# Kernel tuning notes

Hardware: AMD Instinct MI355X
Metric: run time of the kernel (lower is better)

## Reference

```python
import jax, jax.numpy as jnp
import numpy as np

NUM_GROUPS = 32
EPS = 1e-6


def group_norm(x, gamma, beta):
    # x: [B, C, H, W]
    B, C, H, W = x.shape
    xg = x.reshape(B, NUM_GROUPS, C // NUM_GROUPS, H, W)
    mean = jnp.mean(xg, axis=(2, 3, 4), keepdims=True)
    var = jnp.var(xg, axis=(2, 3, 4), keepdims=True)
    xn = (xg - mean) * jax.lax.rsqrt(var + EPS)
    xn = xn.reshape(B, C, H, W)
    return xn * gamma[None, :, None, None] + beta[None, :, None, None]


def conv1x1(x, w, b):
    # x: [B, C, H, W], w: [Cout, Cin], b: [Cout]
    return jnp.einsum('bchw,dc->bdhw', x, w) + b[None, :, None, None]


def setup_inputs() -> dict:
    key = jax.random.key(0)
    ks = jax.random.split(key, 11)
    B, C, H, W = 4, 512, 64, 64
    s = 1.0 / np.sqrt(C)
    return {
        'x': jax.random.normal(ks[0], (B, C, H, W), dtype=jnp.float32),
        'gn_gamma': jnp.ones((C,), dtype=jnp.float32),
        'gn_beta': jnp.zeros((C,), dtype=jnp.float32),
        'wq': jax.random.normal(ks[1], (C, C), dtype=jnp.float32) * s,
        'bq': jax.random.normal(ks[2], (C,), dtype=jnp.float32) * 0.01,
        'wk': jax.random.normal(ks[3], (C, C), dtype=jnp.float32) * s,
        'bk': jax.random.normal(ks[4], (C,), dtype=jnp.float32) * 0.01,
        'wv': jax.random.normal(ks[5], (C, C), dtype=jnp.float32) * s,
        'bv': jax.random.normal(ks[6], (C,), dtype=jnp.float32) * 0.01,
        'wo': jax.random.normal(ks[7], (C, C), dtype=jnp.float32) * s,
        'bo': jax.random.normal(ks[8], (C,), dtype=jnp.float32) * 0.01,
    }


def reference(x, gn_gamma, gn_beta, wq, bq, wk, bk, wv, bv, wo, bo):
    B, C, H, W = x.shape
    h = group_norm(x, gn_gamma, gn_beta)
    q = conv1x1(h, wq, bq).reshape(B, C, H * W)  # [B, C, N]
    k = conv1x1(h, wk, bk).reshape(B, C, H * W)
    v = conv1x1(h, wv, bv).reshape(B, C, H * W)
    scale = jnp.asarray(C, x.dtype) ** -0.5
    # scores[b, i, j] = q_i . k_j
    scores = jnp.einsum('bci,bcj->bij', q, k) * scale  # [B, N, N]
    attn = jax.nn.softmax(scores, axis=2)
    # out[b, c, i] = sum_j v[b, c, j] * attn[b, i, j]
    out = jnp.einsum('bcj,bij->bci', v, attn).reshape(B, C, H, W)
    out = conv1x1(out, wo, bo)
    return x + out
```

## Files before the change

kernel.cpp:

```cpp
#include <hip/hip_runtime.h>

using uint = unsigned int;
typedef short bf16x8 __attribute__((ext_vector_type(8)));
typedef _Float16 f16x8 __attribute__((ext_vector_type(8)));
typedef float f32x4 __attribute__((ext_vector_type(4)));
typedef long i64;
typedef i64 i64x2 __attribute__((ext_vector_type(2)));

static constexpr int Cc = 512;
static constexpr int Nn = 4096;
static constexpr size_t NC = (size_t)Nn * Cc;
static constexpr size_t SN = (size_t)Nn * Nn;

__device__ __forceinline__ unsigned short f2bf(float f) {
    unsigned int u = __builtin_bit_cast(unsigned int, f);
    u = (u + 0x7fff + ((u >> 16) & 1)) >> 16;
    return (unsigned short)u;
}
__device__ __forceinline__ unsigned short f2h(float f) {
    _Float16 h = (_Float16)f;
    return __builtin_bit_cast(unsigned short, h);
}
__device__ __forceinline__ int perm64(int k) {
    return (k & ~63) | ((k & 0x18) << 1) | ((k & 0x20) >> 2) | (k & 7);
}

__device__ __forceinline__ void gll16(const void* g, void* l) {
    __builtin_amdgcn_global_load_lds(
        (const __attribute__((address_space(1))) void*)g,
        (__attribute__((address_space(3))) void*)l, 16, 0, 0);
}

__global__ void cvt_kernel(const float* __restrict__ in, unsigned short* __restrict__ out, int n4) {
    int i = blockIdx.x * blockDim.x + threadIdx.x;
    if (i < n4) {
        float4 v = ((const float4*)in)[i];
        out[i * 4 + 0] = f2bf(v.x);
        out[i * 4 + 1] = f2bf(v.y);
        out[i * 4 + 2] = f2bf(v.z);
        out[i * 4 + 3] = f2bf(v.w);
    }
}

__global__ void zero_kernel(float* __restrict__ p, int n4) {
    int i = blockIdx.x * blockDim.x + threadIdx.x;
    if (i < n4) ((float4*)p)[i] = make_float4(0.f, 0.f, 0.f, 0.f);
}

__global__ void gn_stats_kernel(const float* __restrict__ x, float* __restrict__ meanb,
                                float* __restrict__ rsb) {
    int bg = blockIdx.x;
    const float* slab = x + (size_t)bg * 16 * Nn;
    const float4* s4 = (const float4*)slab;
    int t = threadIdx.x;
    float s1 = 0.f, s2 = 0.f;
#pragma unroll 8
    for (int k = 0; k < 64; ++k) {
        float4 v = s4[k * 256 + t];
        s1 += v.x + v.y + v.z + v.w;
        s2 += v.x * v.x + v.y * v.y + v.z * v.z + v.w * v.w;
    }
#pragma unroll
    for (int o = 32; o > 0; o >>= 1) { s1 += __shfl_down(s1, o); s2 += __shfl_down(s2, o); }
    __shared__ float r1[4], r2[4];
    int wv_ = t >> 6, ln = t & 63;
    if (ln == 0) { r1[wv_] = s1; r2[wv_] = s2; }
    __syncthreads();
    if (t == 0) {
        float a1 = r1[0] + r1[1] + r1[2] + r1[3];
        float a2 = r2[0] + r2[1] + r2[2] + r2[3];
        float mean = a1 * (1.f / 65536.f);
        float var = a2 * (1.f / 65536.f) - mean * mean;
        meanb[bg] = mean;
        rsb[bg] = rsqrtf(var + 1e-6f);
    }
}

__global__ __launch_bounds__(256) void gn_norm_kernel(
    const float* __restrict__ x, const float* __restrict__ meanb, const float* __restrict__ rsb,
    const float* __restrict__ gamma, const float* __restrict__ beta,
    unsigned short* __restrict__ h_t) {
    __shared__ float tile[64][65];
    int n0 = blockIdx.x * 64, c0 = blockIdx.y * 64, b = blockIdx.z;
    int t = threadIdx.x;
    const float* xb = x + (size_t)b * Cc * Nn;
#pragma unroll
    for (int j = 0; j < 4; ++j) {
        int i = j * 256 + t;
        int c = i >> 4;
        int n4 = i & 15;
        int cg = c0 + c;
        float4 v = ((const float4*)(xb + (size_t)cg * Nn + n0))[n4];
        int g = cg >> 4;
        float mean = meanb[b * 32 + g], rs = rsb[b * 32 + g];
        float ga = gamma[cg] * rs;
        float be = beta[cg] - mean * ga;
        tile[n4 * 4 + 0][c] = v.x * ga + be;
        tile[n4 * 4 + 1][c] = v.y * ga + be;
        tile[n4 * 4 + 2][c] = v.z * ga + be;
        tile[n4 * 4 + 3][c] = v.w * ga + be;
    }
    __syncthreads();
    int n = t >> 2;
    int cpart = (t & 3) * 16;
    unsigned short o[16];
#pragma unroll
    for (int q = 0; q < 16; ++q) o[q] = f2bf(tile[n][cpart + q]);
    unsigned short* dst = h_t + (size_t)b * NC + (size_t)(n0 + n) * Cc + c0 + cpart;
    ((uint4*)dst)[0] = ((uint4*)o)[0];
    ((uint4*)dst)[1] = ((uint4*)o)[1];
}

template <int BM, int DT, int BIAS_MODE, int OUT_MODE, int HAS_RES>
__global__ __launch_bounds__(256, 2) void gemm_bt(
    const unsigned short* __restrict__ A, int lda, size_t sA,
    const unsigned short* __restrict__ Bt, int ldb, size_t sB,
    void* __restrict__ outp, int ldc, size_t sC,
    const float* __restrict__ bias,
    const float* __restrict__ res, size_t sR,
    int K, float alpha) {
    constexpr int MT = BM / 32;
    __shared__ unsigned short lA[BM * 64];
    __shared__ unsigned short lB[128 * 64];
    int z = blockIdx.z;
    A += (size_t)z * sA;
    Bt += (size_t)z * sB;
    int m0 = blockIdx.y * BM, n0 = blockIdx.x * 128;
    int t = threadIdx.x;
    int lane = t & 63, wave = t >> 6;
    int wm = wave >> 1, wn = wave & 1;
    int lo = lane & 15, quad = lane >> 4;

    f32x4 acc[MT][4];
#pragma unroll
    for (int a1 = 0; a1 < MT; ++a1)
#pragma unroll
        for (int a2 = 0; a2 < 4; ++a2) acc[a1][a2] = (f32x4){0.f, 0.f, 0.f, 0.f};

    for (int k0 = 0; k0 < K; k0 += 64) {
#pragma unroll
        for (int p = 0; p < MT; ++p) {
            int ci = p * 256 + t;
            int row = ci >> 3;
            int gs = (ci ^ row) & 7;
            gll16(A + (size_t)(m0 + row) * lda + k0 + gs * 8, &lA[(size_t)ci * 8]);
        }
#pragma unroll
        for (int p = 0; p < 4; ++p) {
            int ci = p * 256 + t;
            int row = ci >> 3;
            int gs = (ci ^ row) & 7;
            gll16(Bt + (size_t)(n0 + row) * ldb + k0 + gs * 8, &lB[(size_t)ci * 8]);
        }
        __syncthreads();
#pragma unroll
        for (int ks = 0; ks < 2; ++ks) {
            int G = quad + ks * 4;
            bf16x8 af[MT], bfr[4];
#pragma unroll
            for (int mt = 0; mt < MT; ++mt) {
                int R = wm * (BM / 2) + mt * 16 + lo;
                af[mt] = *(const bf16x8*)&lA[R * 64 + (((G ^ R) & 7) << 3)];
            }
#pragma unroll
            for (int nt = 0; nt < 4; ++nt) {
                int R = wn * 64 + nt * 16 + lo;
                bfr[nt] = *(const bf16x8*)&lB[R * 64 + (((G ^ R) & 7) << 3)];
            }
#pragma unroll
            for (int mt = 0; mt < MT; ++mt)
#pragma unroll
                for (int nt = 0; nt < 4; ++nt) {
                    if (DT == 0)
                        acc[mt][nt] = __builtin_amdgcn_mfma_f32_16x16x32_bf16(af[mt], bfr[nt], acc[mt][nt], 0, 0, 0);
                    else
                        acc[mt][nt] = __builtin_amdgcn_mfma_f32_16x16x32_f16(
                            __builtin_bit_cast(f16x8, af[mt]), __builtin_bit_cast(f16x8, bfr[nt]),
                            acc[mt][nt], 0, 0, 0);
                }
        }
        __syncthreads();
    }

    size_t zc = (size_t)z * sC;
    float* outf = (float*)outp + zc;
    unsigned short* outb = (unsigned short*)outp + zc;
    unsigned char* outc = (unsigned char*)outp + zc;
    const float* resz = HAS_RES ? res + (size_t)z * sR : nullptr;

#pragma unroll
    for (int mt = 0; mt < MT; ++mt) {
#pragma unroll
        for (int nt = 0; nt < 4; ++nt) {
            int row = m0 + wm * (BM / 2) + mt * 16 + quad * 4;
            int col = n0 + wn * 64 + nt * 16 + lo;
            float bn = (BIAS_MODE == 2) ? bias[col] : 0.f;
#pragma unroll
            for (int r = 0; r < 4; ++r) {
                float vv = acc[mt][nt][r];
                if (BIAS_MODE == 1) vv += bias[row + r];
                if (BIAS_MODE == 2) vv += bn;
                vv *= alpha;
                if (OUT_MODE == 3) {
                    float e = fmaxf(fminf(vv, 448.f), -448.f);
                    int pk = __builtin_amdgcn_cvt_pk_fp8_f32(e, e, 0, false);
                    outc[(size_t)(row + r) * ldc + perm64(col)] = (unsigned char)(pk & 0xff);
                } else {
                    size_t off = (size_t)(row + r) * ldc + col;
                    if (HAS_RES) vv += resz[off];
                    if (OUT_MODE == 0) outf[off] = vv;
                    else if (OUT_MODE == 1) outb[off] = f2bf(vv);
                    else outb[off] = f2h(vv);
                }
            }
        }
    }
}

__global__ __launch_bounds__(256, 2) void qk_fp8(
    const unsigned char* __restrict__ Q, const unsigned char* __restrict__ Kt,
    unsigned char* __restrict__ S, float* __restrict__ lsum, float alpha) {
    __shared__ unsigned char lA[256 * 128];
    __shared__ unsigned char lB[128 * 128];
    int z = blockIdx.z;
    Q += (size_t)z * NC;
    Kt += (size_t)z * NC;
    S += (size_t)z * SN;
    lsum += (size_t)z * Nn;
    int m0 = blockIdx.y * 256, n0 = blockIdx.x * 128;
    int t = threadIdx.x;
    int lane = t & 63, wave = t >> 6;
    int wm = wave >> 1, wn = wave & 1;
    int lo = lane & 15, quad = lane >> 4;

    f32x4 acc[8][4];
#pragma unroll
    for (int a1 = 0; a1 < 8; ++a1)
#pragma unroll
        for (int a2 = 0; a2 < 4; ++a2) acc[a1][a2] = (f32x4){0.f, 0.f, 0.f, 0.f};

    for (int k0 = 0; k0 < Cc; k0 += 128) {
#pragma unroll
        for (int p = 0; p < 8; ++p) {
            int ci = p * 256 + t;
            int row = ci >> 3, g = ci & 7;
            int gs = g ^ (row & 7);
            gll16(Q + (size_t)(m0 + row) * Cc + k0 + gs * 16, &lA[ci * 16]);
        }
#pragma unroll
        for (int p = 0; p < 4; ++p) {
            int ci = p * 256 + t;
            int row = ci >> 3, g = ci & 7;
            int gs = g ^ (row & 7);
            gll16(Kt + (size_t)(n0 + row) * Cc + k0 + gs * 16, &lB[ci * 16]);
        }
        __syncthreads();
#pragma unroll
        for (int c = 0; c < 2; ++c) {
            int gb = c * 4 + quad;
            i64x2 aq[8], bq[4];
#pragma unroll
            for (int mt = 0; mt < 8; ++mt) {
                int R = wm * 128 + mt * 16 + lo;
                aq[mt] = *(const i64x2*)&lA[R * 128 + ((gb ^ (R & 7)) << 4)];
            }
#pragma unroll
            for (int nt = 0; nt < 4; ++nt) {
                int R = wn * 64 + nt * 16 + lo;
                bq[nt] = *(const i64x2*)&lB[R * 128 + ((gb ^ (R & 7)) << 4)];
            }
#pragma unroll
            for (int ks = 0; ks < 2; ++ks)
#pragma unroll
                for (int mt = 0; mt < 8; ++mt)
#pragma unroll
                    for (int nt = 0; nt < 4; ++nt)
                        acc[mt][nt] = __builtin_amdgcn_mfma_f32_16x16x32_fp8_fp8(
                            aq[mt][ks], bq[nt][ks], acc[mt][nt], 0, 0, 0);
        }
        __syncthreads();
    }

#pragma unroll
    for (int mt = 0; mt < 8; ++mt) {
        int row = m0 + wm * 128 + mt * 16 + quad * 4;
        float rsum[4] = {0.f, 0.f, 0.f, 0.f};
#pragma unroll
        for (int nt = 0; nt < 4; ++nt) {
            int col = n0 + wn * 64 + nt * 16 + lo;
            int colp = perm64(col);
#pragma unroll
            for (int r = 0; r < 4; ++r) {
                float e = __expf(acc[mt][nt][r] * alpha - 2.f);
                e = fminf(e, 448.f);
                int pk = __builtin_amdgcn_cvt_pk_fp8_f32(e, e, 0, false);
                S[(size_t)(row + r) * Nn + colp] = (unsigned char)(pk & 0xff);
                rsum[r] += __builtin_amdgcn_cvt_f32_fp8(pk, 0);
            }
        }
#pragma unroll
        for (int o = 1; o < 16; o <<= 1) {
#pragma unroll
            for (int r = 0; r < 4; ++r) rsum[r] += __shfl_xor(rsum[r], o);
        }
        if (lo == 0) {
#pragma unroll
            for (int r = 0; r < 4; ++r) atomicAdd(&lsum[row + r], rsum[r]);
        }
    }
}

__global__ __launch_bounds__(256, 3) void pv_fp8(
    const unsigned char* __restrict__ S, const unsigned char* __restrict__ V,
    const float* __restrict__ lsum, unsigned short* __restrict__ o_t) {
    __shared__ unsigned char lA[128 * 128];
    __shared__ unsigned char lB[128 * 128];
    int z = blockIdx.z;
    S += (size_t)z * SN;
    V += (size_t)z * NC;
    lsum += (size_t)z * Nn;
    o_t += (size_t)z * NC;
    int m0 = blockIdx.y * 128, n0 = blockIdx.x * 128;
    int t = threadIdx.x;
    int lane = t & 63, wave = t >> 6;
    int wm = wave >> 1, wn = wave & 1;
    int lo = lane & 15, quad = lane >> 4;

    f32x4 acc[4][4];
#pragma unroll
    for (int a1 = 0; a1 < 4; ++a1)
#pragma unroll
        for (int a2 = 0; a2 < 4; ++a2) acc[a1][a2] = (f32x4){0.f, 0.f, 0.f, 0.f};

    for (int k0 = 0; k0 < Nn; k0 += 128) {
#pragma unroll
        for (int p = 0; p < 4; ++p) {
            int ci = p * 256 + t;
            int row = ci >> 3, g = ci & 7;
            int gs = g ^ (row & 7);
            gll16(S + (size_t)(m0 + row) * Nn + k0 + gs * 16, &lA[ci * 16]);
        }
#pragma unroll
        for (int p = 0; p < 4; ++p) {
            int ci = p * 256 + t;
            int row = ci >> 3, g = ci & 7;
            int gs = g ^ (row & 7);
            gll16(V + (size_t)(n0 + row) * Nn + k0 + gs * 16, &lB[ci * 16]);
        }
        __syncthreads();
#pragma unroll
        for (int c = 0; c < 2; ++c) {
            int gb = c * 4 + quad;
            i64x2 aq[4], bq[4];
#pragma unroll
            for (int mt = 0; mt < 4; ++mt) {
                int R = wm * 64 + mt * 16 + lo;
                aq[mt] = *(const i64x2*)&lA[R * 128 + ((gb ^ (R & 7)) << 4)];
            }
#pragma unroll
            for (int nt = 0; nt < 4; ++nt) {
                int R = wn * 64 + nt * 16 + lo;
                bq[nt] = *(const i64x2*)&lB[R * 128 + ((gb ^ (R & 7)) << 4)];
            }
#pragma unroll
            for (int ks = 0; ks < 2; ++ks)
#pragma unroll
                for (int mt = 0; mt < 4; ++mt)
#pragma unroll
                    for (int nt = 0; nt < 4; ++nt)
                        acc[mt][nt] = __builtin_amdgcn_mfma_f32_16x16x32_fp8_fp8(
                            aq[mt][ks], bq[nt][ks], acc[mt][nt], 0, 0, 0);
        }
        __syncthreads();
    }

#pragma unroll
    for (int mt = 0; mt < 4; ++mt)
#pragma unroll
        for (int nt = 0; nt < 4; ++nt) {
            int row = m0 + wm * 64 + mt * 16 + quad * 4;
            int col = n0 + wn * 64 + nt * 16 + lo;
#pragma unroll
            for (int r = 0; r < 4; ++r) {
                float vv = acc[mt][nt][r] / lsum[row + r];
                o_t[(size_t)(row + r) * Cc + col] = f2bf(vv);
            }
        }
}

extern "C" void kernel_launch(void* const* d_in, const int* in_sizes, int n_in,
                              void* d_out, int out_size, void* d_ws, size_t ws_size,
                              hipStream_t stream) {
    const float* x     = (const float*)d_in[0];
    const float* gamma = (const float*)d_in[1];
    const float* beta  = (const float*)d_in[2];
    const float* wq = (const float*)d_in[3];
    const float* bq = (const float*)d_in[4];
    const float* wk = (const float*)d_in[5];
    const float* bk = (const float*)d_in[6];
    const float* wv = (const float*)d_in[7];
    const float* bv = (const float*)d_in[8];
    const float* wo = (const float*)d_in[9];
    const float* bo = (const float*)d_in[10];

    char* ws = (char*)d_ws;
    unsigned short* h_t  = (unsigned short*)(ws);
    unsigned char*  q_8  = (unsigned char*)(ws + 16777216);
    unsigned char*  k_8  = (unsigned char*)(ws + 33554432);
    unsigned char*  v_8  = (unsigned char*)(ws + 50331648);
    unsigned short* o_t  = (unsigned short*)(ws + 67108864);
    unsigned char*  S    = (unsigned char*)(ws + 83886080);
    unsigned short* wqb  = (unsigned short*)(ws + 218103808);
    unsigned short* wkb  = (unsigned short*)(ws + 218628096);
    unsigned short* wvb  = (unsigned short*)(ws + 219152384);
    unsigned short* wob  = (unsigned short*)(ws + 219676672);
    float* statm         = (float*)(ws + 220200960);
    float* statr         = (float*)(ws + 220201984);
    float* lsum          = (float*)(ws + 220203008);

    const float SCALE = 0.044194173824159216f;

    cvt_kernel<<<256, 256, 0, stream>>>(wq, wqb, 65536);
    cvt_kernel<<<256, 256, 0, stream>>>(wk, wkb, 65536);
    cvt_kernel<<<256, 256, 0, stream>>>(wv, wvb, 65536);
    cvt_kernel<<<256, 256, 0, stream>>>(wo, wob, 65536);
    zero_kernel<<<16, 256, 0, stream>>>(lsum, 4096);

    gn_stats_kernel<<<128, 256, 0, stream>>>(x, statm, statr);
    gn_norm_kernel<<<dim3(64, 8, 4), 256, 0, stream>>>(x, statm, statr, gamma, beta, h_t);

    gemm_bt<128, 0, 2, 3, 0><<<dim3(4, 32, 4), 256, 0, stream>>>(
        h_t, Cc, NC, wqb, Cc, 0, q_8, Cc, NC, bq, nullptr, 0, Cc, 1.f);
    gemm_bt<128, 0, 2, 3, 0><<<dim3(4, 32, 4), 256, 0, stream>>>(
        h_t, Cc, NC, wkb, Cc, 0, k_8, Cc, NC, bk, nullptr, 0, Cc, 1.f);
    gemm_bt<128, 0, 1, 3, 0><<<dim3(32, 4, 4), 256, 0, stream>>>(
        wvb, Cc, 0, h_t, Cc, NC, v_8, Nn, NC, bv, nullptr, 0, Cc, 1.f);

    qk_fp8<<<dim3(32, 16, 4), 256, 0, stream>>>(q_8, k_8, S, lsum, SCALE);
    pv_fp8<<<dim3(4, 32, 4), 256, 0, stream>>>(S, v_8, lsum, o_t);

    gemm_bt<128, 0, 1, 0, 1><<<dim3(32, 4, 4), 256, 0, stream>>>(
        wob, Cc, 0, o_t, Cc, NC, d_out, Nn, NC, bo, x, NC, Cc, 1.f);
}
```

Baseline: 314.9 us.

## Double-buffer LDS tiles in GEMM, QK and PV kernels to overlap loads

Converts the three matmul kernels to a two-stage LDS ping-pong: the next K-slice is issued via global-to-LDS loads while MFMAs run on the current buffer. The fp8 kernels shrink the K step from 128 to 64 bytes per stage so total LDS stays roughly the same, with a new XOR swizzle over 4 chunks. The aim is to hide global load latency behind compute. In exchange it doubles the iteration count and barrier count in the fp8 kernels, and the GEMM's LDS use doubles, which may reduce occupancy.

```diff
diff --git a/kernel.cpp b/kernel.cpp
--- a/kernel.cpp
+++ b/kernel.cpp
@@ -120,8 +120,8 @@
     const float* __restrict__ res, size_t sR,
     int K, float alpha) {
     constexpr int MT = BM / 32;
-    __shared__ unsigned short lA[BM * 64];
-    __shared__ unsigned short lB[128 * 64];
+    __shared__ unsigned short lA[2][BM * 64];
+    __shared__ unsigned short lB[2][128 * 64];
     int z = blockIdx.z;
     A += (size_t)z * sA;
     Bt += (size_t)z * sB;
@@ -137,22 +137,29 @@
 #pragma unroll
         for (int a2 = 0; a2 < 4; ++a2) acc[a1][a2] = (f32x4){0.f, 0.f, 0.f, 0.f};
 
-    for (int k0 = 0; k0 < K; k0 += 64) {
+    auto stage = [&](int buf, int k0) {
 #pragma unroll
         for (int p = 0; p < MT; ++p) {
             int ci = p * 256 + t;
             int row = ci >> 3;
             int gs = (ci ^ row) & 7;
-            gll16(A + (size_t)(m0 + row) * lda + k0 + gs * 8, &lA[(size_t)ci * 8]);
+            gll16(A + (size_t)(m0 + row) * lda + k0 + gs * 8, &lA[buf][ci * 8]);
         }
 #pragma unroll
         for (int p = 0; p < 4; ++p) {
             int ci = p * 256 + t;
             int row = ci >> 3;
             int gs = (ci ^ row) & 7;
-            gll16(Bt + (size_t)(n0 + row) * ldb + k0 + gs * 8, &lB[(size_t)ci * 8]);
-        }
-        __syncthreads();
+            gll16(Bt + (size_t)(n0 + row) * ldb + k0 + gs * 8, &lB[buf][ci * 8]);
+        }
+    };
+
+    int nk = K >> 6;
+    stage(0, 0);
+    __syncthreads();
+    int cur = 0;
+    for (int it = 0; it < nk; ++it) {
+        if (it + 1 < nk) stage(cur ^ 1, (it + 1) << 6);
 #pragma unroll
         for (int ks = 0; ks < 2; ++ks) {
             int G = quad + ks * 4;
@@ -160,12 +167,12 @@
 #pragma unroll
             for (int mt = 0; mt < MT; ++mt) {
                 int R = wm * (BM / 2) + mt * 16 + lo;
-                af[mt] = *(const bf16x8*)&lA[R * 64 + (((G ^ R) & 7) << 3)];
+                af[mt] = *(const bf16x8*)&lA[cur][R * 64 + (((G ^ R) & 7) << 3)];
             }
 #pragma unroll
             for (int nt = 0; nt < 4; ++nt) {
                 int R = wn * 64 + nt * 16 + lo;
-                bfr[nt] = *(const bf16x8*)&lB[R * 64 + (((G ^ R) & 7) << 3)];
+                bfr[nt] = *(const bf16x8*)&lB[cur][R * 64 + (((G ^ R) & 7) << 3)];
             }
 #pragma unroll
             for (int mt = 0; mt < MT; ++mt)
@@ -180,6 +187,7 @@
                 }
         }
         __syncthreads();
+        cur ^= 1;
     }
 
     size_t zc = (size_t)z * sC;
@@ -220,8 +228,8 @@
 __global__ __launch_bounds__(256, 2) void qk_fp8(
     const unsigned char* __restrict__ Q, const unsigned char* __restrict__ Kt,
     unsigned char* __restrict__ S, float* __restrict__ lsum, float alpha) {
-    __shared__ unsigned char lA[256 * 128];
-    __shared__ unsigned char lB[128 * 128];
+    __shared__ unsigned char lA[2][256 * 64];
+    __shared__ unsigned char lB[2][128 * 64];
     int z = blockIdx.z;
     Q += (size_t)z * NC;
     Kt += (size_t)z * NC;
@@ -239,46 +247,49 @@
 #pragma unroll
         for (int a2 = 0; a2 < 4; ++a2) acc[a1][a2] = (f32x4){0.f, 0.f, 0.f, 0.f};
 
-    for (int k0 = 0; k0 < Cc; k0 += 128) {
-#pragma unroll
-        for (int p = 0; p < 8; ++p) {
-            int ci = p * 256 + t;
-            int row = ci >> 3, g = ci & 7;
-            int gs = g ^ (row & 7);
-            gll16(Q + (size_t)(m0 + row) * Cc + k0 + gs * 16, &lA[ci * 16]);
-        }
+    auto stage = [&](int buf, int k0) {
 #pragma unroll
         for (int p = 0; p < 4; ++p) {
             int ci = p * 256 + t;
-            int row = ci >> 3, g = ci & 7;
-            int gs = g ^ (row & 7);
-            gll16(Kt + (size_t)(n0 + row) * Cc + k0 + gs * 16, &lB[ci * 16]);
-        }
+            int row = ci >> 2;
+            int gs = (ci ^ row) & 3;
+            gll16(Q + (size_t)(m0 + row) * Cc + k0 + gs * 16, &lA[buf][ci * 16]);
+        }
+#pragma unroll
+        for (int p = 0; p < 2; ++p) {
+            int ci = p * 256 + t;
+            int row = ci >> 2;
+            int gs = (ci ^ row) & 3;
+            gll16(Kt + (size_t)(n0 + row) * Cc + k0 + gs * 16, &lB[buf][ci * 16]);
+        }
+    };
+
+    stage(0, 0);
+    __syncthreads();
+    int cur = 0;
+    for (int it = 0; it < 8; ++it) {
+        if (it < 7) stage(cur ^ 1, (it + 1) * 64);
+        i64x2 aq[8], bq[4];
+#pragma unroll
+        for (int mt = 0; mt < 8; ++mt) {
+            int R = wm * 128 + mt * 16 + lo;
+            aq[mt] = *(const i64x2*)&lA[cur][R * 64 + ((quad ^ (R & 3)) << 4)];
+        }
+#pragma unroll
+        for (int nt = 0; nt < 4; ++nt) {
+            int R = wn * 64 + nt * 16 + lo;
+            bq[nt] = *(const i64x2*)&lB[cur][R * 64 + ((quad ^ (R & 3)) << 4)];
+        }
+#pragma unroll
+        for (int ks = 0; ks < 2; ++ks)
+#pragma unroll
+            for (int mt = 0; mt < 8; ++mt)
+#pragma unroll
+                for (int nt = 0; nt < 4; ++nt)
+                    acc[mt][nt] = __builtin_amdgcn_mfma_f32_16x16x32_fp8_fp8(
+                        aq[mt][ks], bq[nt][ks], acc[mt][nt], 0, 0, 0);
         __syncthreads();
-#pragma unroll
-        for (int c = 0; c < 2; ++c) {
-            int gb = c * 4 + quad;
-            i64x2 aq[8], bq[4];
-#pragma unroll
-            for (int mt = 0; mt < 8; ++mt) {
-                int R = wm * 128 + mt * 16 + lo;
-                aq[mt] = *(const i64x2*)&lA[R * 128 + ((gb ^ (R & 7)) << 4)];
-            }
-#pragma unroll
-            for (int nt = 0; nt < 4; ++nt) {
-                int R = wn * 64 + nt * 16 + lo;
-                bq[nt] = *(const i64x2*)&lB[R * 128 + ((gb ^ (R & 7)) << 4)];
-            }
-#pragma unroll
-            for (int ks = 0; ks < 2; ++ks)
-#pragma unroll
-                for (int mt = 0; mt < 8; ++mt)
-#pragma unroll
-                    for (int nt = 0; nt < 4; ++nt)
-                        acc[mt][nt] = __builtin_amdgcn_mfma_f32_16x16x32_fp8_fp8(
-                            aq[mt][ks], bq[nt][ks], acc[mt][nt], 0, 0, 0);
-        }
-        __syncthreads();
+        cur ^= 1;
     }
 
 #pragma unroll
@@ -313,8 +324,8 @@
 __global__ __launch_bounds__(256, 3) void pv_fp8(
     const unsigned char* __restrict__ S, const unsigned char* __restrict__ V,
     const float* __restrict__ lsum, unsigned short* __restrict__ o_t) {
-    __shared__ unsigned char lA[128 * 128];
-    __shared__ unsigned char lB[128 * 128];
+    __shared__ unsigned char lA[2][128 * 64];
+    __shared__ unsigned char lB[2][128 * 64];
     int z = blockIdx.z;
     S += (size_t)z * SN;
     V += (size_t)z * NC;
@@ -332,46 +343,49 @@
 #pragma unroll
         for (int a2 = 0; a2 < 4; ++a2) acc[a1][a2] = (f32x4){0.f, 0.f, 0.f, 0.f};
 
-    for (int k0 = 0; k0 < Nn; k0 += 128) {
-#pragma unroll
-        for (int p = 0; p < 4; ++p) {
-            int ci = p * 256 + t;
-            int row = ci >> 3, g = ci & 7;
-            int gs = g ^ (row & 7);
-            gll16(S + (size_t)(m0 + row) * Nn + k0 + gs * 16, &lA[ci * 16]);
-        }
-#pragma unroll
-        for (int p = 0; p < 4; ++p) {
-            int ci = p * 256 + t;
-            int row = ci >> 3, g = ci & 7;
-            int gs = g ^ (row & 7);
-            gll16(V + (size_t)(n0 + row) * Nn + k0 + gs * 16, &lB[ci * 16]);
-        }
+    auto stage = [&](int buf, int k0) {
+#pragma unroll
+        for (int p = 0; p < 2; ++p) {
+            int ci = p * 256 + t;
+            int row = ci >> 2;
+            int gs = (ci ^ row) & 3;
+            gll16(S + (size_t)(m0 + row) * Nn + k0 + gs * 16, &lA[buf][ci * 16]);
+        }
+#pragma unroll
+        for (int p = 0; p < 2; ++p) {
+            int ci = p * 256 + t;
+            int row = ci >> 2;
+            int gs = (ci ^ row) & 3;
+            gll16(V + (size_t)(n0 + row) * Nn + k0 + gs * 16, &lB[buf][ci * 16]);
+        }
+    };
+
+    stage(0, 0);
+    __syncthreads();
+    int cur = 0;
+    for (int it = 0; it < 64; ++it) {
+        if (it < 63) stage(cur ^ 1, (it + 1) * 64);
+        i64x2 aq[4], bq[4];
+#pragma unroll
+        for (int mt = 0; mt < 4; ++mt) {
+            int R = wm * 64 + mt * 16 + lo;
+            aq[mt] = *(const i64x2*)&lA[cur][R * 64 + ((quad ^ (R & 3)) << 4)];
+        }
+#pragma unroll
+        for (int nt = 0; nt < 4; ++nt) {
+            int R = wn * 64 + nt * 16 + lo;
+            bq[nt] = *(const i64x2*)&lB[cur][R * 64 + ((quad ^ (R & 3)) << 4)];
+        }
+#pragma unroll
+        for (int ks = 0; ks < 2; ++ks)
+#pragma unroll
+            for (int mt = 0; mt < 4; ++mt)
+#pragma unroll
+                for (int nt = 0; nt < 4; ++nt)
+                    acc[mt][nt] = __builtin_amdgcn_mfma_f32_16x16x32_fp8_fp8(
+                        aq[mt][ks], bq[nt][ks], acc[mt][nt], 0, 0, 0);
         __syncthreads();
-#pragma unroll
-        for (int c = 0; c < 2; ++c) {
-            int gb = c * 4 + quad;
-            i64x2 aq[4], bq[4];
-#pragma unroll
-            for (int mt = 0; mt < 4; ++mt) {
-                int R = wm * 64 + mt * 16 + lo;
-                aq[mt] = *(const i64x2*)&lA[R * 128 + ((gb ^ (R & 7)) << 4)];
-            }
-#pragma unroll
-            for (int nt = 0; nt < 4; ++nt) {
-                int R = wn * 64 + nt * 16 + lo;
-                bq[nt] = *(const i64x2*)&lB[R * 128 + ((gb ^ (R & 7)) << 4)];
-            }
-#pragma unroll
-            for (int ks = 0; ks < 2; ++ks)
-#pragma unroll
-                for (int mt = 0; mt < 4; ++mt)
-#pragma unroll
-                    for (int nt = 0; nt < 4; ++nt)
-                        acc[mt][nt] = __builtin_amdgcn_mfma_f32_16x16x32_fp8_fp8(
-                            aq[mt][ks], bq[nt][ks], acc[mt][nt], 0, 0, 0);
-        }
-        __syncthreads();
+        cur ^= 1;
     }
 
 #pragma unroll
```

New measurement: 337.9 us. +7.3%, slower.
